# Kernel optimization log

Measured on AMD Instinct MI355X. Metric: run time of the kernel, lower is better.

The kernel has to match this reference:

```python
import math
import jax, jax.numpy as jnp
import numpy as np

STRATEGY = 'small'
K_PEAKS = 2
BW = math.radians(15.0)
HIGH_RATIO = 0.3
LOW_RATIO = 0.2
ALPHA = 1.2
BETA = 0.8
N_BINS = 180


def setup_inputs() -> dict:
    key = jax.random.key(0)
    k1, k2, k3 = jax.random.split(key, 3)
    x = jax.random.normal(k1, (16, 256, 128, 128), dtype=jnp.float32)
    w_in = jax.random.normal(k2, (16, 256), dtype=jnp.float32) * 0.06    # proj_in 1x1 conv weight [c_mid, C]
    w_out = jax.random.normal(k3, (256, 16), dtype=jnp.float32) * 0.25   # proj_out 1x1 conv weight [C, c_mid]
    return {"x": x, "w_in": w_in, "w_out": w_out}


def _forward(x, w_in, w_out):
    B, C, H, W = x.shape
    pi = jnp.float32(math.pi)
    cy, cx = H // 2, W // 2
    y = jnp.arange(H, dtype=jnp.float32)[:, None]
    xg = jnp.arange(W, dtype=jnp.float32)[None, :]
    r = jnp.sqrt((y - cy) ** 2 + (xg - cx) ** 2)                 # [H, W]
    theta = jnp.arctan2(y - cy, xg - cx) + pi                    # [H, W] in [0, 2pi]
    r_max = float(min(cy, cx))

    # 1x1 conv in
    x_proj = jnp.einsum('mc,bchw->bmhw', w_in, x)                # [B, c_mid, H, W]

    fs = jnp.fft.fftshift(jnp.fft.fft2(x_proj, norm='ortho'), axes=(-2, -1))
    mag = jnp.abs(fs)                                            # [B, c_mid, H, W]

    # ---- peak direction detection (180-bin angular histogram of high-freq energy) ----
    theta_mod = theta % pi
    high_mask = (r > HIGH_RATIO * r_max).astype(jnp.float32)     # [H, W]
    bin_edges = jnp.linspace(0.0, math.pi, N_BINS + 1, dtype=jnp.float32)
    mag_avg = mag.mean(axis=1)                                   # [B, H, W]
    weighted = (mag_avg * high_mask).reshape(B, -1)              # [B, H*W]
    bin_idx = jnp.clip(jnp.searchsorted(bin_edges, theta_mod.reshape(-1), side='left') - 1, 0, N_BINS - 1)
    energy = jax.vmap(lambda w: jax.ops.segment_sum(w, bin_idx, num_segments=N_BINS))(weighted)  # [B, 180]

    # smooth with [0.25, 0.5, 0.25], zero padding
    ep = jnp.pad(energy, ((0, 0), (1, 1)))
    es = 0.25 * ep[:, :-2] + 0.5 * ep[:, 1:-1] + 0.25 * ep[:, 2:]  # [B, 180]

    mean_e = es.mean(axis=-1, keepdims=True)
    is_peak = (es > mean_e) & (es > jnp.roll(es, 1, axis=-1)) & (es > jnp.roll(es, -1, axis=-1))
    vals = jnp.where(is_peak, es, -jnp.inf)
    topv, topi = jax.lax.top_k(vals, K_PEAKS)                    # [B, k]
    count = jnp.sum(topv > -jnp.inf, axis=-1)                    # [B] number of valid peaks (<= k)
    amax = jnp.argmax(es, axis=-1)                               # fallback when no peak found
    topi = jnp.where((count > 0)[:, None], topi, amax[:, None])
    eff = jnp.maximum(count, 1)
    pos = jnp.minimum(jnp.arange(K_PEAKS)[None, :], (eff - 1)[:, None])  # pad with last valid peak
    final_idx = jnp.take_along_axis(topi, pos, axis=1)           # [B, k]
    bin_center = (bin_edges[:-1] + bin_edges[1:]) * 0.5
    peak_angles = bin_center[final_idx]                          # [B, k]

    # ---- gain map (channel-independent) ----
    if STRATEGY == 'small':
        pa = peak_angles
        base_mask = high_mask
    else:
        pa = (peak_angles + pi / 2) % pi
        base_mask = (r <= LOW_RATIO * r_max).astype(jnp.float32)
    diff = jnp.abs(theta[None, None] - pa[:, :, None, None])     # [B, k, H, W]
    diff = jnp.minimum(diff, pi - diff)
    in_region = (diff <= BW) & (base_mask[None, None] > 0)
    enh = jnp.any(in_region, axis=1).astype(jnp.float32)         # [B, H, W]
    gain = jnp.where(enh > 0, jnp.float32(ALPHA), jnp.float32(1.0))
    other_high = high_mask[None] * (1.0 - enh)
    gain = gain * (1.0 - other_high) + other_high * BETA         # [B, H, W]

    fs_enh = fs * gain[:, None, :, :]
    x_enh = jnp.fft.ifft2(jnp.fft.ifftshift(fs_enh, axes=(-2, -1)), norm='ortho').real
    out = jnp.einsum('cm,bmhw->bchw', w_out, x_enh)
    return x + out


def reference(x, w_in, w_out):
    return _forward(x, w_in, w_out)
```

## Files before the change

kernel.cpp:

```cpp
#include <hip/hip_runtime.h>
#include <math.h>

#define NPX 16384

static constexpr float  PI_F   = 3.14159265358979323846f;
static constexpr double PI_D   = 3.14159265358979323846;
static constexpr double STEP_D = PI_D / 180.0;
static constexpr double BW_D   = 15.0 * (PI_D / 180.0);

typedef float f4 __attribute__((ext_vector_type(4)));
typedef float f2 __attribute__((ext_vector_type(2)));

__device__ __forceinline__ int swz(int r, int c) {
    return (r << 7) | (c ^ (r ^ (r >> 1)));
}
__device__ __forceinline__ int brev7(int x) { return (int)(__brev((unsigned)x) >> 25); }
__device__ __forceinline__ float2 cadd(float2 a, float2 b){ return make_float2(a.x+b.x, a.y+b.y); }
__device__ __forceinline__ float2 csub(float2 a, float2 b){ return make_float2(a.x-b.x, a.y-b.y); }
__device__ __forceinline__ float2 cmul(float2 a, float re, float im){
    return make_float2(a.x*re - a.y*im, a.x*im + a.y*re);
}
__device__ __forceinline__ double edge_d(int i) {
    return (i >= 180) ? PI_D : (double)i * STEP_D;
}

__global__ void k0_tables(double* __restrict__ theta_s, int* __restrict__ bin_s,
                          double* __restrict__ energy) {
    int p = blockIdx.x * blockDim.x + threadIdx.x;
    if (p < NPX) {
        int r = p >> 7, c = p & 127;
        int pix = ((brev7(r) ^ 64) << 7) | (brev7(c) ^ 64);
        int h = pix >> 7, w = pix & 127;
        double dy = (double)(h - 64), dx = (double)(w - 64);
        double theta = atan2(dy, dx) + PI_D;
        theta_s[p] = theta;
        double v = fmod(theta, PI_D);
        int cnt = 0;
        for (int i = 0; i <= 180; ++i) cnt += (edge_d(i) < v) ? 1 : 0;
        int bin = cnt - 1;
        if (bin < 0) bin = 0;
        if (bin > 179) bin = 179;
        int r2 = (h - 64)*(h - 64) + (w - 64)*(w - 64);
        bool high = (r2 >= 369);
        bin_s[p] = high ? bin : -1;
    }
    if (blockIdx.x == 0) {
        for (int i = threadIdx.x; i < 16 * 180; i += blockDim.x) energy[i] = 0.0;
    }
}

__global__ __launch_bounds__(256, 1) void k1_proj(const float* __restrict__ x,
        const float* __restrict__ w_in, float* __restrict__ xpp) {
    int b = blockIdx.y, z = blockIdx.z;
    int t4 = blockIdx.x * blockDim.x + threadIdx.x;
    const f4* xb = (const f4*)(x + ((size_t)b * 256 + (size_t)z * 128) * NPX);
    f4 acc[16];
    #pragma unroll
    for (int m = 0; m < 16; ++m) acc[m] = (f4)0.0f;
    #pragma unroll 16
    for (int c = 0; c < 128; ++c) {
        f4 xv = __builtin_nontemporal_load(&xb[(size_t)c * (NPX/4) + t4]);
        #pragma unroll
        for (int m = 0; m < 16; ++m) {
            float wv = w_in[m * 256 + z * 128 + c];
            acc[m] += wv * xv;
        }
    }
    f4* xp = (f4*)xpp + ((size_t)z * 256 + b * 16) * (NPX/4);
    #pragma unroll
    for (int m = 0; m < 16; ++m) xp[(size_t)m * (NPX/4) + t4] = acc[m];
}

__global__ __launch_bounds__(1024) void k_fft_fwd(const float* __restrict__ xpp,
        float2* __restrict__ fs, const int* __restrict__ bin_s,
        double* __restrict__ energy) {
    extern __shared__ float2 lds[];
    __shared__ float twr[64], twi[64];
    __shared__ double histp[8][180];
    const int tid = threadIdx.x;
    const int img = blockIdx.x;
    if (tid < 64) {
        float ang = (float)tid * (PI_F / 64.0f);
        twr[tid] = cosf(ang);
        twi[tid] = sinf(ang);
    }
    if (tid < 180) {
        #pragma unroll
        for (int g = 0; g < 8; ++g) histp[g][tid] = 0.0;
    }
    const f4* s0 = (const f4*)xpp + (size_t)img * (NPX/4);
    const f4* s1 = (const f4*)xpp + (size_t)(256 + img) * (NPX/4);
    #pragma unroll
    for (int it = 0; it < 4; ++it) {
        int p4 = tid + it * 1024;
        f4 v = s0[p4] + s1[p4];
        int pb = p4 * 4;
        #pragma unroll
        for (int j = 0; j < 4; ++j) {
            int p = pb + j;
            lds[swz(p >> 7, p & 127)] = make_float2(v[j], 0.0f);
        }
    }
    __syncthreads();
    #pragma unroll
    for (int dim = 0; dim < 2; ++dim) {
        #pragma unroll
        for (int s = 0; s <= 4; s += 2) {
            const int q = 32 >> s;
            #pragma unroll
            for (int it = 0; it < 4; ++it) {
                int fb = tid + it * 1024;
                int o = fb & 127;
                int bfi = fb >> 7;
                int p = bfi & (q - 1);
                int g = bfi >> (5 - s);
                int P = g * (128 >> s) + p;
                int k1 = p << s;
                float tc = twr[k1],   ts = twi[k1];
                float uc = twr[2*k1], us = twi[2*k1];
                int e0, e1, e2, e3;
                if (dim == 0) { e0=swz(o,P); e1=swz(o,P+q); e2=swz(o,P+2*q); e3=swz(o,P+3*q); }
                else          { e0=swz(P,o); e1=swz(P+q,o); e2=swz(P+2*q,o); e3=swz(P+3*q,o); }
                float2 a = lds[e0], b = lds[e1], c = lds[e2], d = lds[e3];
                float2 u0 = cadd(a, c);
                float2 u1 = cmul(csub(a, c), tc, -ts);
                float2 v0 = cadd(b, d);
                float2 v1 = cmul(csub(b, d), -ts, -tc);
                lds[e0] = cadd(u0, v0);
                lds[e1] = cmul(csub(u0, v0), uc, -us);
                lds[e2] = cadd(u1, v1);
                lds[e3] = cmul(csub(u1, v1), uc, -us);
            }
            __syncthreads();
        }
        #pragma unroll
        for (int it = 0; it < 8; ++it) {
            int fb = tid + it * 1024;
            int o = fb & 127;
            int g = fb >> 7;
            int e0, e1;
            if (dim == 0) { e0 = swz(o, 2*g); e1 = swz(o, 2*g+1); }
            else          { e0 = swz(2*g, o); e1 = swz(2*g+1, o); }
            float2 a = lds[e0], b = lds[e1];
            lds[e0] = cadd(a, b);
            lds[e1] = csub(a, b);
        }
        __syncthreads();
    }
    float2* dst = fs + (size_t)img * NPX;
    const int bofs = (img >> 4) * 180;
    const int grp = tid >> 7;
    #pragma unroll
    for (int it = 0; it < 16; ++it) {
        int p = tid + it * 1024;
        int r = p >> 7, c = p & 127;
        float2 v = lds[swz(r, c)];
        dst[p] = v;
        int bh = bin_s[p];
        if (bh >= 0) {
            double m = sqrt((double)v.x * (double)v.x + (double)v.y * (double)v.y);
            atomicAdd(&histp[grp][bh], m);
        }
    }
    __syncthreads();
    if (tid < 180) {
        double s = 0.0;
        #pragma unroll
        for (int g = 0; g < 8; ++g) s += histp[g][tid];
        atomicAdd(&energy[bofs + tid], s);
    }
}

__global__ void k3_peaks(const double* __restrict__ energy, const double* __restrict__ theta_s,
                         const int* __restrict__ bin_s, float* __restrict__ gain_s) {
    __shared__ double e[180], es[180];
    __shared__ double pa[2];
    int b = blockIdx.x, tid = threadIdx.x;
    if (tid < 180) e[tid] = energy[b * 180 + tid];
    __syncthreads();
    if (tid < 180) {
        double l = (tid > 0)   ? e[tid-1] : 0.0;
        double r = (tid < 179) ? e[tid+1] : 0.0;
        es[tid] = 0.25*l + 0.5*e[tid] + 0.25*r;
    }
    __syncthreads();
    if (tid == 0) {
        double sum = 0.0;
        for (int i = 0; i < 180; ++i) sum += es[i];
        double mean = sum / 180.0;
        double v0 = -INFINITY, v1 = -INFINITY;
        int   i0 = -1, i1 = -1;
        for (int i = 0; i < 180; ++i) {
            double prev = es[(i + 179) % 180];
            double nxt  = es[(i + 1) % 180];
            bool pk = (es[i] > mean) && (es[i] > prev) && (es[i] > nxt);
            if (pk) {
                double v = es[i];
                if (v > v0)      { v1 = v0; i1 = i0; v0 = v; i0 = i; }
                else if (v > v1) { v1 = v;  i1 = i; }
            }
        }
        int idx0, idx1;
        if (i0 < 0) {
            double mv = es[0]; int mi = 0;
            for (int i = 1; i < 180; ++i) if (es[i] > mv) { mv = es[i]; mi = i; }
            idx0 = idx1 = mi;
        } else if (i1 < 0) { idx0 = idx1 = i0; }
        else               { idx0 = i0; idx1 = i1; }
        pa[0] = (edge_d(idx0) + edge_d(idx0 + 1)) * 0.5;
        pa[1] = (edge_d(idx1) + edge_d(idx1 + 1)) * 0.5;
    }
    __syncthreads();
    double pa0 = pa[0], pa1 = pa[1];
    for (int p = tid; p < NPX; p += blockDim.x) {
        double th = theta_s[p];
        bool high = bin_s[p] >= 0;
        double d0 = fabs(th - pa0); d0 = fmin(d0, PI_D - d0);
        double d1 = fabs(th - pa1); d1 = fmin(d1, PI_D - d1);
        bool enh = ((d0 <= BW_D) || (d1 <= BW_D)) && high;
        float g = enh ? 1.2f : (high ? 0.8f : 1.0f);
        gain_s[(size_t)b * NPX + p] = g * (1.0f / 16384.0f);
    }
}

__global__ __launch_bounds__(1024) void k_fft_inv(const float2* __restrict__ fs,
        const float* __restrict__ gain_s, float* __restrict__ xe) {
    extern __shared__ float2 lds[];
    __shared__ float twr[64], twi[64];
    const int tid = threadIdx.x;
    const int img = blockIdx.x;
    if (tid < 64) {
        float ang = (float)tid * (PI_F / 64.0f);
        twr[tid] = cosf(ang);
        twi[tid] = sinf(ang);
    }
    const f4* srcv = (const f4*)(fs + (size_t)img * NPX);
    const f2* gbv  = (const f2*)(gain_s + (size_t)(img >> 4) * NPX);
    #pragma unroll
    for (int it = 0; it < 8; ++it) {
        int q = tid + it * 1024;
        f4 v = srcv[q];
        f2 g = gbv[q];
        int p = q * 2;
        lds[swz(p >> 7, p & 127)]             = make_float2(v.x * g.x, v.y * g.x);
        lds[swz((p+1) >> 7, (p+1) & 127)]     = make_float2(v.z * g.y, v.w * g.y);
    }
    __syncthreads();
    #pragma unroll
    for (int dim = 0; dim < 2; ++dim) {
        #pragma unroll
        for (int it = 0; it < 8; ++it) {
            int fb = tid + it * 1024;
            int o = fb & 127;
            int g = fb >> 7;
            int e0, e1;
            if (dim == 0) { e0 = swz(o, 2*g); e1 = swz(o, 2*g+1); }
            else          { e0 = swz(2*g, o); e1 = swz(2*g+1, o); }
            float2 a = lds[e0], b = lds[e1];
            lds[e0] = cadd(a, b);
            lds[e1] = csub(a, b);
        }
        __syncthreads();
        #pragma unroll
        for (int s = 4; s >= 0; s -= 2) {
            const int q = 32 >> s;
            #pragma unroll
            for (int it = 0; it < 4; ++it) {
                int fb = tid + it * 1024;
                int o = fb & 127;
                int bfi = fb >> 7;
                int p = bfi & (q - 1);
                int g = bfi >> (5 - s);
                int P = g * (128 >> s) + p;
                int k1 = p << s;
                float tc = twr[k1],   ts = twi[k1];
                float uc = twr[2*k1], us = twi[2*k1];
                int e0, e1, e2, e3;
                if (dim == 0) { e0=swz(o,P); e1=swz(o,P+q); e2=swz(o,P+2*q); e3=swz(o,P+3*q); }
                else          { e0=swz(P,o); e1=swz(P+q,o); e2=swz(P+2*q,o); e3=swz(P+3*q,o); }
                float2 o0 = lds[e0], o1 = lds[e1], o2 = lds[e2], o3 = lds[e3];
                float2 t1 = cmul(o1, uc, us);
                float2 u0 = cadd(o0, t1);
                float2 v0 = csub(o0, t1);
                float2 t3 = cmul(o3, uc, us);
                float2 u1 = cadd(o2, t3);
                float2 v1 = csub(o2, t3);
                float2 ta = cmul(u1, tc, ts);
                float2 tb = cmul(v1, -ts, tc);
                lds[e0] = cadd(u0, ta);
                lds[e2] = csub(u0, ta);
                lds[e1] = cadd(v0, tb);
                lds[e3] = csub(v0, tb);
            }
            __syncthreads();
        }
    }
    float* dstx = xe + (size_t)img * NPX;
    #pragma unroll
    for (int it = 0; it < 16; ++it) {
        int p = tid + it * 1024;
        dstx[p] = lds[swz(p >> 7, p & 127)].x;
    }
}

__global__ __launch_bounds__(256, 1) void k5_out(const float* __restrict__ x,
        const float* __restrict__ w_out, const float* __restrict__ xe,
        float* __restrict__ out) {
    int b = blockIdx.z, ct = blockIdx.y, pt = blockIdx.x, t = threadIdx.x;
    int p4 = pt * 256 + t;
    const f4* xeb = (const f4*)(xe + (size_t)b * 16 * NPX);
    f4 xv[16];
    #pragma unroll
    for (int m = 0; m < 16; ++m) xv[m] = xeb[(size_t)m * (NPX/4) + p4];
    #pragma unroll 8
    for (int cc = 0; cc < 16; ++cc) {
        int c = ct * 16 + cc;
        size_t base = ((size_t)b * 256 + c) * NPX;
        f4 a = __builtin_nontemporal_load((const f4*)(x + base) + p4);
        #pragma unroll
        for (int m = 0; m < 16; ++m) {
            float wv = w_out[c * 16 + m];
            a += wv * xv[m];
        }
        __builtin_nontemporal_store(a, (f4*)(out + base) + p4);
    }
}

extern "C" void kernel_launch(void* const* d_in, const int* in_sizes, int n_in,
                              void* d_out, int out_size, void* d_ws, size_t ws_size,
                              hipStream_t stream) {
    const float* x     = (const float*)d_in[0];
    const float* w_in  = (const float*)d_in[1];
    const float* w_out = (const float*)d_in[2];
    float* out = (float*)d_out;
    char* ws = (char*)d_ws;

    double* theta_s = (double*)(ws);
    int*    bin_s   = (int*)   (ws + 0x20000);
    double* energy  = (double*)(ws + 0x30000);
    float*  gain_s  = (float*) (ws + 0x40000);
    float*  xe      = (float*) (ws + 0x140000);
    float*  xpp = (float*)((char*)d_out + ((size_t)128 << 20));
    float2* fs  = (float2*)((char*)d_out + ((size_t)224 << 20));

    (void)hipFuncSetAttribute((const void*)k_fft_fwd,
            hipFuncAttributeMaxDynamicSharedMemorySize, 131072);
    (void)hipFuncSetAttribute((const void*)k_fft_inv,
            hipFuncAttributeMaxDynamicSharedMemorySize, 131072);

    k0_tables<<<dim3(64), dim3(256), 0, stream>>>(theta_s, bin_s, energy);
    k1_proj  <<<dim3(16, 16, 2), dim3(256), 0, stream>>>(x, w_in, xpp);
    k_fft_fwd<<<dim3(256), dim3(1024), 131072, stream>>>(xpp, fs, bin_s, energy);
    k3_peaks <<<dim3(16), dim3(256), 0, stream>>>(energy, theta_s, bin_s, gain_s);
    k_fft_inv<<<dim3(256), dim3(1024), 131072, stream>>>(fs, gain_s, xe);
    k5_out   <<<dim3(16, 16, 16), dim3(256), 0, stream>>>(x, w_out, xe, out);
}
```

Measured before the change: 246.8 us.

## Fuse peak detection and gain computation into inverse FFT kernel

Removes the separate k3_peaks kernel and the gain_s buffer. Each inverse-FFT block now redoes the histogram smoothing and peak search for its batch and computes the per-pixel gain on the fly while loading spectrum data, prefetching the spectrum before that serial step. This saves one launch and the gain map write and read, but repeats the single-thread peak search 16 times per batch and adds double-precision gain math to every block. It also fully unrolls the channel loop in k5_out.

```diff
diff --git a/kernel.cpp b/kernel.cpp
--- a/kernel.cpp
+++ b/kernel.cpp
@@ -171,12 +171,27 @@
     }
 }
 
-__global__ void k3_peaks(const double* __restrict__ energy, const double* __restrict__ theta_s,
-                         const int* __restrict__ bin_s, float* __restrict__ gain_s) {
+__global__ __launch_bounds__(1024) void k_fft_inv(const float2* __restrict__ fs,
+        const double* __restrict__ energy, const double* __restrict__ theta_s,
+        const int* __restrict__ bin_s, float* __restrict__ xe) {
+    extern __shared__ float2 lds[];
+    __shared__ float twr[64], twi[64];
     __shared__ double e[180], es[180];
     __shared__ double pa[2];
-    int b = blockIdx.x, tid = threadIdx.x;
-    if (tid < 180) e[tid] = energy[b * 180 + tid];
+    const int tid = threadIdx.x;
+    const int img = blockIdx.x;
+    const int bofs = (img >> 4) * 180;
+    if (tid < 64) {
+        float ang = (float)tid * (PI_F / 64.0f);
+        twr[tid] = cosf(ang);
+        twi[tid] = sinf(ang);
+    }
+    const f4* srcv = (const f4*)(fs + (size_t)img * NPX);
+    f4 v0 = srcv[tid],        v1 = srcv[tid + 1024];
+    f4 v2 = srcv[tid + 2048], v3 = srcv[tid + 3072];
+    f4 v4 = srcv[tid + 4096], v5 = srcv[tid + 5120];
+    f4 v6 = srcv[tid + 6144], v7 = srcv[tid + 7168];
+    if (tid < 180) e[tid] = energy[bofs + tid];
     __syncthreads();
     if (tid < 180) {
         double l = (tid > 0)   ? e[tid-1] : 0.0;
@@ -188,7 +203,7 @@
         double sum = 0.0;
         for (int i = 0; i < 180; ++i) sum += es[i];
         double mean = sum / 180.0;
-        double v0 = -INFINITY, v1 = -INFINITY;
+        double w0 = -INFINITY, w1 = -INFINITY;
         int   i0 = -1, i1 = -1;
         for (int i = 0; i < 180; ++i) {
             double prev = es[(i + 179) % 180];
@@ -196,8 +211,8 @@
             bool pk = (es[i] > mean) && (es[i] > prev) && (es[i] > nxt);
             if (pk) {
                 double v = es[i];
-                if (v > v0)      { v1 = v0; i1 = i0; v0 = v; i0 = i; }
-                else if (v > v1) { v1 = v;  i1 = i; }
+                if (v > w0)      { w1 = w0; i1 = i0; w0 = v; i0 = i; }
+                else if (v > w1) { w1 = v;  i1 = i; }
             }
         }
         int idx0, idx1;
@@ -211,40 +226,27 @@
         pa[1] = (edge_d(idx1) + edge_d(idx1 + 1)) * 0.5;
     }
     __syncthreads();
-    double pa0 = pa[0], pa1 = pa[1];
-    for (int p = tid; p < NPX; p += blockDim.x) {
-        double th = theta_s[p];
-        bool high = bin_s[p] >= 0;
-        double d0 = fabs(th - pa0); d0 = fmin(d0, PI_D - d0);
-        double d1 = fabs(th - pa1); d1 = fmin(d1, PI_D - d1);
-        bool enh = ((d0 <= BW_D) || (d1 <= BW_D)) && high;
-        float g = enh ? 1.2f : (high ? 0.8f : 1.0f);
-        gain_s[(size_t)b * NPX + p] = g * (1.0f / 16384.0f);
-    }
-}
-
-__global__ __launch_bounds__(1024) void k_fft_inv(const float2* __restrict__ fs,
-        const float* __restrict__ gain_s, float* __restrict__ xe) {
-    extern __shared__ float2 lds[];
-    __shared__ float twr[64], twi[64];
-    const int tid = threadIdx.x;
-    const int img = blockIdx.x;
-    if (tid < 64) {
-        float ang = (float)tid * (PI_F / 64.0f);
-        twr[tid] = cosf(ang);
-        twi[tid] = sinf(ang);
-    }
-    const f4* srcv = (const f4*)(fs + (size_t)img * NPX);
-    const f2* gbv  = (const f2*)(gain_s + (size_t)(img >> 4) * NPX);
-    #pragma unroll
-    for (int it = 0; it < 8; ++it) {
-        int q = tid + it * 1024;
-        f4 v = srcv[q];
-        f2 g = gbv[q];
-        int p = q * 2;
-        lds[swz(p >> 7, p & 127)]             = make_float2(v.x * g.x, v.y * g.x);
-        lds[swz((p+1) >> 7, (p+1) & 127)]     = make_float2(v.z * g.y, v.w * g.y);
-    }
+    const double pa0 = pa[0], pa1 = pa[1];
+    #define GAIN_PUT(vv, qq) {                                                        \
+        int p0 = (qq) * 2;                                                            \
+        _Pragma("unroll")                                                             \
+        for (int j = 0; j < 2; ++j) {                                                 \
+            int p = p0 + j;                                                           \
+            double th = theta_s[p];                                                   \
+            bool high = bin_s[p] >= 0;                                                \
+            double d0 = fabs(th - pa0); d0 = fmin(d0, PI_D - d0);                     \
+            double d1 = fabs(th - pa1); d1 = fmin(d1, PI_D - d1);                     \
+            bool enh = ((d0 <= BW_D) || (d1 <= BW_D)) && high;                        \
+            float g = (enh ? 1.2f : (high ? 0.8f : 1.0f)) * (1.0f / 16384.0f);        \
+            lds[swz(p >> 7, p & 127)] =                                               \
+                make_float2(vv[2*j] * g, vv[2*j + 1] * g);                            \
+        }                                                                             \
+    }
+    GAIN_PUT(v0, tid)        GAIN_PUT(v1, tid + 1024)
+    GAIN_PUT(v2, tid + 2048) GAIN_PUT(v3, tid + 3072)
+    GAIN_PUT(v4, tid + 4096) GAIN_PUT(v5, tid + 5120)
+    GAIN_PUT(v6, tid + 6144) GAIN_PUT(v7, tid + 7168)
+    #undef GAIN_PUT
     __syncthreads();
     #pragma unroll
     for (int dim = 0; dim < 2; ++dim) {
@@ -281,16 +283,16 @@
                 float2 o0 = lds[e0], o1 = lds[e1], o2 = lds[e2], o3 = lds[e3];
                 float2 t1 = cmul(o1, uc, us);
                 float2 u0 = cadd(o0, t1);
-                float2 v0 = csub(o0, t1);
+                float2 w0 = csub(o0, t1);
                 float2 t3 = cmul(o3, uc, us);
                 float2 u1 = cadd(o2, t3);
-                float2 v1 = csub(o2, t3);
+                float2 w1 = csub(o2, t3);
                 float2 ta = cmul(u1, tc, ts);
-                float2 tb = cmul(v1, -ts, tc);
+                float2 tb = cmul(w1, -ts, tc);
                 lds[e0] = cadd(u0, ta);
                 lds[e2] = csub(u0, ta);
-                lds[e1] = cadd(v0, tb);
-                lds[e3] = csub(v0, tb);
+                lds[e1] = cadd(w0, tb);
+                lds[e3] = csub(w0, tb);
             }
             __syncthreads();
         }
@@ -312,7 +314,7 @@
     f4 xv[16];
     #pragma unroll
     for (int m = 0; m < 16; ++m) xv[m] = xeb[(size_t)m * (NPX/4) + p4];
-    #pragma unroll 8
+    #pragma unroll
     for (int cc = 0; cc < 16; ++cc) {
         int c = ct * 16 + cc;
         size_t base = ((size_t)b * 256 + c) * NPX;
@@ -338,7 +340,6 @@
     double* theta_s = (double*)(ws);
     int*    bin_s   = (int*)   (ws + 0x20000);
     double* energy  = (double*)(ws + 0x30000);
-    float*  gain_s  = (float*) (ws + 0x40000);
     float*  xe      = (float*) (ws + 0x140000);
     float*  xpp = (float*)((char*)d_out + ((size_t)128 << 20));
     float2* fs  = (float2*)((char*)d_out + ((size_t)224 << 20));
@@ -351,7 +352,6 @@
     k0_tables<<<dim3(64), dim3(256), 0, stream>>>(theta_s, bin_s, energy);
     k1_proj  <<<dim3(16, 16, 2), dim3(256), 0, stream>>>(x, w_in, xpp);
     k_fft_fwd<<<dim3(256), dim3(1024), 131072, stream>>>(xpp, fs, bin_s, energy);
-    k3_peaks <<<dim3(16), dim3(256), 0, stream>>>(energy, theta_s, bin_s, gain_s);
-    k_fft_inv<<<dim3(256), dim3(1024), 131072, stream>>>(fs, gain_s, xe);
+    k_fft_inv<<<dim3(256), dim3(1024), 131072, stream>>>(fs, energy, theta_s, bin_s, xe);
     k5_out   <<<dim3(16, 16, 16), dim3(256), 0, stream>>>(x, w_out, xe, out);
 }
```

Result: no change. 247.0 us (+0.1%).
